# Kernel tuning notes

Hardware: AMD Instinct MI355X
Metric: run time of the kernel (lower is better)

Reference implementation:

```python
import jax, jax.numpy as jnp
import numpy as np

QLEN, MLEN, BSZ = 1024, 1024, 2
D_MODEL, N_HEAD, D_HEAD, D_INNER = 1024, 16, 64, 4096
KLEN = QLEN + MLEN
RLEN = KLEN + QLEN
EPS = 1e-12
SCALE = 1.0 / np.sqrt(D_HEAD).astype(np.float32)
STD = 0.02


def gelu(x):
    # OpenAI-GPT tanh-approx gelu used by XLNet
    return 0.5 * x * (1.0 + jnp.tanh(np.sqrt(2.0 / np.pi) * (x + 0.044715 * x ** 3)))


def layer_norm(x, g, b):
    m = jnp.mean(x, axis=-1, keepdims=True)
    v = jnp.mean((x - m) ** 2, axis=-1, keepdims=True)
    return (x - m) * jax.lax.rsqrt(v + EPS) * g + b


def rel_shift(x, klen):
    # x: [qlen, rlen, bsz, n_head] -> [qlen, klen, bsz, n_head]
    q, r, b, n = x.shape
    x = jnp.reshape(x, (r, q, b, n))[1:]
    x = jnp.reshape(x, (q, r - 1, b, n))[:, :klen]
    return x


def setup_inputs() -> dict:
    key = jax.random.key(0)
    ks = jax.random.split(key, 16)
    h = jax.random.normal(ks[0], (QLEN, BSZ, D_MODEL), jnp.float32)
    mems = jax.random.normal(ks[1], (MLEN, BSZ, D_MODEL), jnp.float32)
    r = jax.random.normal(ks[2], (RLEN, BSZ, D_MODEL), jnp.float32)
    # segment one-hot: 1 if query and key segments differ (XLNet convention)
    qseg = jax.random.randint(ks[3], (QLEN, BSZ), 0, 2)
    kseg = jax.random.randint(ks[4], (KLEN, BSZ), 0, 2)
    seg_mat = jax.nn.one_hot((qseg[:, None, :] != kseg[None, :, :]).astype(jnp.int32), 2, dtype=jnp.float32)  # [q,k,b,2]
    # causal mask with mems: query i may attend to key j <= i + MLEN
    i = jnp.arange(QLEN)[:, None]
    j = jnp.arange(KLEN)[None, :]
    attn_mask = (j > i + MLEN).astype(jnp.float32)[:, :, None, None]  # [q,k,1,1]
    wq = jax.random.normal(ks[5], (D_MODEL, N_HEAD, D_HEAD), jnp.float32) * STD
    wk = jax.random.normal(ks[6], (D_MODEL, N_HEAD, D_HEAD), jnp.float32) * STD
    wv = jax.random.normal(ks[7], (D_MODEL, N_HEAD, D_HEAD), jnp.float32) * STD
    wo = jax.random.normal(ks[8], (D_MODEL, N_HEAD, D_HEAD), jnp.float32) * STD
    wr = jax.random.normal(ks[9], (D_MODEL, N_HEAD, D_HEAD), jnp.float32) * STD
    r_w_bias = jnp.zeros((N_HEAD, D_HEAD), jnp.float32)
    r_r_bias = jnp.zeros((N_HEAD, D_HEAD), jnp.float32)
    r_s_bias = jnp.zeros((N_HEAD, D_HEAD), jnp.float32)
    seg_embed = jax.random.normal(ks[10], (2, N_HEAD, D_HEAD), jnp.float32) * STD
    ln_attn_g = jnp.ones((D_MODEL,), jnp.float32)
    ln_attn_b = jnp.zeros((D_MODEL,), jnp.float32)
    w1 = jax.random.normal(ks[11], (D_MODEL, D_INNER), jnp.float32) * STD
    b1 = jnp.zeros((D_INNER,), jnp.float32)
    w2 = jax.random.normal(ks[12], (D_INNER, D_MODEL), jnp.float32) * STD
    b2 = jnp.zeros((D_MODEL,), jnp.float32)
    ln_ff_g = jnp.ones((D_MODEL,), jnp.float32)
    ln_ff_b = jnp.zeros((D_MODEL,), jnp.float32)
    return dict(h=h, mems=mems, r=r, seg_mat=seg_mat, attn_mask=attn_mask,
                wq=wq, wk=wk, wv=wv, wo=wo, wr=wr,
                r_w_bias=r_w_bias, r_r_bias=r_r_bias, r_s_bias=r_s_bias, seg_embed=seg_embed,
                ln_attn_g=ln_attn_g, ln_attn_b=ln_attn_b,
                w1=w1, b1=b1, w2=w2, b2=b2, ln_ff_g=ln_ff_g, ln_ff_b=ln_ff_b)


def reference(h, mems, r, seg_mat, attn_mask, wq, wk, wv, wo, wr,
              r_w_bias, r_r_bias, r_s_bias, seg_embed,
              ln_attn_g, ln_attn_b, w1, b1, w2, b2, ln_ff_g, ln_ff_b):
    # content-stream XLNet relative attention (g=None path) + FFN
    cat = jnp.concatenate([mems, h], axis=0)            # [klen,b,h]
    q_h = jnp.einsum('ibh,hnd->ibnd', h, wq)
    k_h = jnp.einsum('ibh,hnd->ibnd', cat, wk)
    v_h = jnp.einsum('ibh,hnd->ibnd', cat, wv)
    k_r = jnp.einsum('ibh,hnd->ibnd', r, wr)
    ac = jnp.einsum('ibnd,jbnd->ijbn', q_h + r_w_bias, k_h)
    bd = jnp.einsum('ibnd,jbnd->ijbn', q_h + r_r_bias, k_r)
    bd = rel_shift(bd, KLEN)
    ef = jnp.einsum('ibnd,snd->ibns', q_h + r_s_bias, seg_embed)
    ef = jnp.einsum('ijbs,ibns->ijbn', seg_mat, ef)
    attn_score = (ac + bd + ef) * SCALE - 1e30 * attn_mask
    attn_prob = jax.nn.softmax(attn_score, axis=1)
    attn_vec = jnp.einsum('ijbn,jbnd->ibnd', attn_prob, v_h)
    attn_out = jnp.einsum('ibnd,hnd->ibh', attn_vec, wo) + h
    out_h = layer_norm(attn_out, ln_attn_g, ln_attn_b)
    ff = gelu(out_h @ w1 + b1) @ w2 + b2
    return layer_norm(ff + out_h, ln_ff_g, ln_ff_b)
```

## Files before the change

### kernel.cpp

```cpp
#include <hip/hip_runtime.h>
#include <hip/hip_bf16.h>


#define QLEN 1024
#define MLEN 1024
#define DM 1024
#define NH 16
#define DH 64
#define DI 4096
#define KLEN 2048
#define RLEN 3072

typedef __attribute__((ext_vector_type(8))) short s16x8;
typedef __attribute__((ext_vector_type(4))) float f32x4;
typedef unsigned short us;

__device__ __forceinline__ float bf2f(us u) {
    union { unsigned int i; float f; } x; x.i = ((unsigned int)u) << 16; return x.f;
}
__device__ __forceinline__ us f2bf(float f) {
    union { float f; unsigned int i; } x; x.f = f;
    return (us)((x.i + 0x7fffu + ((x.i >> 16) & 1u)) >> 16);
}
__device__ __forceinline__ void gload16(const void* g, void* lds) {
    __builtin_amdgcn_global_load_lds(
        (const __attribute__((address_space(1))) unsigned int*)g,
        (__attribute__((address_space(3))) unsigned int*)lds, 16, 0, 0);
}

template<bool ISMAX>
__device__ __forceinline__ float block_reduce(float v, float* red, int t) {
    #pragma unroll
    for (int off = 32; off > 0; off >>= 1) {
        float o = __shfl_down(v, off);
        v = ISMAX ? fmaxf(v, o) : (v + o);
    }
    if ((t & 63) == 0) red[t >> 6] = v;
    __syncthreads();
    if (t == 0) {
        float s = red[0];
        #pragma unroll
        for (int w = 1; w < 4; ++w) s = ISMAX ? fmaxf(s, red[w]) : (s + red[w]);
        red[4] = s;
    }
    __syncthreads();
    return red[4];
}

__global__ __launch_bounds__(256) void prep_k(
    const float* __restrict__ mems, const float* __restrict__ h,
    const float* __restrict__ r, const float* __restrict__ wo,
    const float* __restrict__ wq, const float* __restrict__ wk,
    const float* __restrict__ wv, const float* __restrict__ wr,
    const float* __restrict__ w1, const float* __restrict__ w2,
    const float* __restrict__ seg,
    us* __restrict__ cat_bf, us* __restrict__ r_bf, us* __restrict__ wo_b,
    us* __restrict__ wqkv_t, us* __restrict__ wr_t,
    us* __restrict__ w1_t, us* __restrict__ w2_t, us* __restrict__ ksb)
{
    __shared__ us tbuf[64][65];
    int bid = blockIdx.x;
    const int tid = threadIdx.x;
    if (bid < 5632) {
        int t = bid * 256 + tid;
        const float* src; us* dst; int off;
        if (t < 262144)       { src = mems; dst = cat_bf;           off = t; }
        else if (t < 524288)  { src = h;    dst = cat_bf + 2097152; off = t - 262144; }
        else if (t < 1310720) { src = r;    dst = r_bf;             off = t - 524288; }
        else                  { src = wo;   dst = wo_b;             off = t - 1310720; }
        const float4* p = (const float4*)src + 2 * (size_t)off;
        float4 a = p[0], b = p[1];
        us o[8] = { f2bf(a.x), f2bf(a.y), f2bf(a.z), f2bf(a.w),
                    f2bf(b.x), f2bf(b.y), f2bf(b.z), f2bf(b.w) };
        *((uint4*)dst + off) = *(const uint4*)o;
        return;
    }
    bid -= 5632;
    if (bid >= 3072) {
        int t = (bid - 3072) * 256 + tid;
        int bb = t >> 11, j = t & 2047;
        ksb[t] = f2bf(seg[(size_t)j * 4 + bb * 2 + 1]);
        return;
    }
    const float* in; us* out; int R, C, c0, r0;
    if (bid < 1024) {
        int z = bid >> 8, u = bid & 255;
        in  = (z == 0) ? wq : (z == 1) ? wk : (z == 2) ? wv : wr;
        out = (z < 3) ? (wqkv_t + (size_t)z * 1048576) : wr_t;
        R = 1024; C = 1024; c0 = (u & 15) * 64; r0 = (u >> 4) * 64;
    } else if (bid < 2048) {
        int u = bid - 1024;
        in = w1; out = w1_t; R = 1024; C = 4096;
        c0 = (u & 63) * 64; r0 = (u >> 6) * 64;
    } else {
        int u = bid - 2048;
        in = w2; out = w2_t; R = 4096; C = 1024;
        c0 = (u & 15) * 64; r0 = (u >> 4) * 64;
    }
    #pragma unroll
    for (int u = 0; u < 16; ++u) {
        int idx = tid + 256 * u;
        int rr = idx >> 6, cc = idx & 63;
        tbuf[cc][rr] = f2bf(in[(size_t)(r0 + rr) * C + c0 + cc]);
    }
    __syncthreads();
    #pragma unroll
    for (int u = 0; u < 16; ++u) {
        int idx = tid + 256 * u;
        int rr = idx >> 6, cc = idx & 63;
        out[(size_t)(c0 + rr) * R + r0 + cc] = tbuf[rr][cc];
    }
}

__device__ __forceinline__ int offe(int r, int c) {
    return ((r >> 4) * 2 + (c >> 5)) * 512 + (r & 15) * 32 + ((c & 31) ^ ((r & 8) ? 16 : 0));
}

template<int EPI>
__device__ __forceinline__ void gemm8_core(
    const us* __restrict__ A, const us* __restrict__ Bt,
    const float* __restrict__ bias, void* __restrict__ Cout,
    int N, int K, int kbeg, size_t zoff, bool zfirst,
    int bx, int by, us* __restrict__ As8, us* __restrict__ Bs8)
{
    const int tid = threadIdx.x;
    const int w = tid >> 6, l = tid & 63;
    const int lm = l & 15, lg = l >> 4;
    const int wm = w >> 2, wn = w & 3;
    const int m0 = by * 256, n0 = bx * 256;

    int srow[2], scol[2];
    #pragma unroll
    for (int u = 0; u < 2; ++u) {
        int sub = w * 2 + u;
        srow[u] = (sub >> 1) * 16 + (l >> 2);
        scol[u] = (sub & 1) * 32 + (((l & 3) * 8) ^ ((l & 32) ? 16 : 0));
    }

    auto stagePart = [&](int kt1, int P, int db) {
        const us* src = (P < 2) ? (A + (size_t)(m0 + P * 128) * K)
                                : (Bt + (size_t)(n0 + (P - 2) * 128) * K);
        us* dst = ((P < 2) ? As8 : Bs8) + (db * 2 + (P & 1)) * 8192;
        int kc = kbeg + kt1 * 64;
        #pragma unroll
        for (int u = 0; u < 2; ++u)
            gload16(src + (size_t)srow[u] * K + kc + scol[u], dst + (w * 2 + u) * 512);
    };

    f32x4 acc[8][4] = {};
    s16x8 rA0[4][2], rA1[4][2], rB[2][2];

    stagePart(0, 0, 0); stagePart(0, 1, 0); stagePart(0, 2, 0); stagePart(0, 3, 0);

    for (int kt = 0; kt < 16; ++kt) {
        const int d = kt & 1;
        asm volatile("s_waitcnt vmcnt(0)" ::: "memory");
        __builtin_amdgcn_s_barrier();
        asm volatile("" ::: "memory");
        const bool hn = (kt + 1 < 16);
        const us* Ab = As8 + (d * 2 + wm) * 8192;
        const us* Bb = Bs8 + (d * 2 + (wn >> 1)) * 8192;

        if (hn) stagePart(kt + 1, 0, d ^ 1);
        #pragma unroll
        for (int mf2 = 0; mf2 < 4; ++mf2)
            #pragma unroll
            for (int kk = 0; kk < 2; ++kk)
                rA0[mf2][kk] = *(const s16x8*)&Ab[offe(mf2 * 16 + lm, kk * 32 + lg * 8)];
        #pragma unroll
        for (int nf2 = 0; nf2 < 2; ++nf2)
            #pragma unroll
            for (int kk = 0; kk < 2; ++kk)
                rB[nf2][kk] = *(const s16x8*)&Bb[offe((wn & 1) * 64 + nf2 * 16 + lm, kk * 32 + lg * 8)];
        __builtin_amdgcn_s_setprio(1);
        #pragma unroll
        for (int mf2 = 0; mf2 < 4; ++mf2)
            #pragma unroll
            for (int nf2 = 0; nf2 < 2; ++nf2)
                #pragma unroll
                for (int kk = 0; kk < 2; ++kk)
                    acc[mf2][nf2] = __builtin_amdgcn_mfma_f32_16x16x32_bf16(
                        rA0[mf2][kk], rB[nf2][kk], acc[mf2][nf2], 0, 0, 0);
        __builtin_amdgcn_s_setprio(0);

        if (hn) stagePart(kt + 1, 1, d ^ 1);
        #pragma unroll
        for (int mf2 = 0; mf2 < 4; ++mf2)
            #pragma unroll
            for (int kk = 0; kk < 2; ++kk)
                rA1[mf2][kk] = *(const s16x8*)&Ab[offe(64 + mf2 * 16 + lm, kk * 32 + lg * 8)];
        __builtin_amdgcn_s_setprio(1);
        #pragma unroll
        for (int mf2 = 0; mf2 < 4; ++mf2)
            #pragma unroll
            for (int nf2 = 0; nf2 < 2; ++nf2)
                #pragma unroll
                for (int kk = 0; kk < 2; ++kk)
                    acc[4 + mf2][nf2] = __builtin_amdgcn_mfma_f32_16x16x32_bf16(
                        rA1[mf2][kk], rB[nf2][kk], acc[4 + mf2][nf2], 0, 0, 0);
        __builtin_amdgcn_s_setprio(0);

        if (hn) stagePart(kt + 1, 2, d ^ 1);
        #pragma unroll
        for (int nf2 = 0; nf2 < 2; ++nf2)
            #pragma unroll
            for (int kk = 0; kk < 2; ++kk)
                rB[nf2][kk] = *(const s16x8*)&Bb[offe((wn & 1) * 64 + (2 + nf2) * 16 + lm, kk * 32 + lg * 8)];
        __builtin_amdgcn_s_setprio(1);
        #pragma unroll
        for (int mf2 = 0; mf2 < 4; ++mf2)
            #pragma unroll
            for (int nf2 = 0; nf2 < 2; ++nf2)
                #pragma unroll
                for (int kk = 0; kk < 2; ++kk)
                    acc[4 + mf2][2 + nf2] = __builtin_amdgcn_mfma_f32_16x16x32_bf16(
                        rA1[mf2][kk], rB[nf2][kk], acc[4 + mf2][2 + nf2], 0, 0, 0);
        __builtin_amdgcn_s_setprio(0);

        if (hn) stagePart(kt + 1, 3, d ^ 1);
        __builtin_amdgcn_s_setprio(1);
        #pragma unroll
        for (int mf2 = 0; mf2 < 4; ++mf2)
            #pragma unroll
            for (int nf2 = 0; nf2 < 2; ++nf2)
                #pragma unroll
                for (int kk = 0; kk < 2; ++kk)
                    acc[mf2][2 + nf2] = __builtin_amdgcn_mfma_f32_16x16x32_bf16(
                        rA0[mf2][kk], rB[nf2][kk], acc[mf2][2 + nf2], 0, 0, 0);
        __builtin_amdgcn_s_setprio(0);
    }

    #pragma unroll
    for (int mf = 0; mf < 8; ++mf) {
        #pragma unroll
        for (int nf = 0; nf < 4; ++nf) {
            #pragma unroll
            for (int rr = 0; rr < 4; ++rr) {
                int row = m0 + wm * 128 + mf * 16 + lg * 4 + rr;
                int col = n0 + wn * 64 + nf * 16 + lm;
                float v = acc[mf][nf][rr];
                if (EPI == 3) {
                    int s = row >> 1, bb = row & 1, nn = col >> 6, dd = col & 63;
                    if (s >= 1) {
                        int g = (s - 1) >> 4, lmw = (s - 1) & 15;
                        int ks2 = dd >> 5, lg2 = (dd >> 3) & 3, e2 = dd & 7;
                        ((us*)Cout)[((((size_t)(bb * 16 + nn)) * 144 + g) * 2 + ks2) * 512
                                    + (lg2 * 16 + lmw) * 8 + e2] = f2bf(v);
                    }
                } else {
                    int which = col >> 10;
                    int nn = (col >> 6) & 15, dd = col & 63, bb = row & 1;
                    us val = f2bf(v);
                    us* base = (us*)Cout;
                    if (which == 0) {
                        if (row >= 2048)
                            base[(((size_t)(bb * 16 + nn)) * 1024 + ((row - 2048) >> 1)) * 64 + dd] = val;
                    } else if (which == 1) {
                        int j = row >> 1;
                        int jt = j >> 6, ff = (j >> 4) & 3, lmw = j & 15;
                        int ks2 = dd >> 5, lg2 = (dd >> 3) & 3, e2 = dd & 7;
                        (base + 2097152)[((((size_t)(bb * 16 + nn)) * 32 + jt) * 8 + ff * 2 + ks2) * 512
                                         + (lg2 * 16 + lmw) * 8 + e2] = val;
                    } else {
                        int j = row >> 1;
                        int jt = j >> 6, ks2 = (j >> 5) & 1, lg2 = (j >> 3) & 3, e2 = j & 7;
                        int df = dd >> 4, lmw = dd & 15;
                        (base + 6291456)[((((size_t)(bb * 16 + nn)) * 32 + jt) * 8 + df * 2 + ks2) * 512
                                         + (lg2 * 16 + lmw) * 8 + e2] = val;
                    }
                }
            }
        }
    }
}

__global__ __launch_bounds__(512) void proj8_k(
    const us* __restrict__ cat_bf, const us* __restrict__ wqkv_t,
    const us* __restrict__ r_bf, const us* __restrict__ wr_t,
    us* __restrict__ qkv_out, us* __restrict__ krf_out)
{
    __shared__ __align__(16) us As8[2 * 2 * 8192];
    __shared__ __align__(16) us Bs8[2 * 2 * 8192];
    int bid = blockIdx.x;
    if (bid < 192) {
        int swz = (bid & 7) * 24 + (bid >> 3);
        gemm8_core<4>(cat_bf, wqkv_t, nullptr, qkv_out, 3072, 1024, 0,
                      0, true, swz % 12, swz / 12, As8, Bs8);
    } else {
        int idx = bid - 192;
        gemm8_core<3>(r_bf, wr_t, nullptr, krf_out, 1024, 1024, 0,
                      0, true, idx & 3, idx >> 2, As8, Bs8);
    }
}

template<int TM, int EPI>
__device__ __forceinline__ void gemm_core(
    const us* __restrict__ A, const us* __restrict__ Bt,
    const float* __restrict__ bias, void* __restrict__ Cout,
    int N, int K, int kbeg, int kchunk, size_t zoff, bool zfirst,
    int bx, int by, us* __restrict__ As, us* __restrict__ Bs)
{
    constexpr int MF = TM / 32;
    constexpr int AISS = TM / 64;
    const int tid = threadIdx.x;
    const int w = tid >> 6, l = tid & 63;
    const int lm = l & 15, lg = l >> 4;
    const int m0 = by * TM, n0 = bx * 128;
    const int wr = (w >> 1) * (TM / 2), wc = (w & 1) * 64;
    const int nt = kchunk / 32;

    f32x4 acc[MF][4] = {};

    auto stage = [&](int buf, int k0) {
        #pragma unroll
        for (int u = 0; u < AISS; ++u) {
            int c = (u * 4 + w) * 64 + l;
            int row = c & (TM - 1), kc = c >> (TM == 128 ? 7 : 6);
            gload16(A + (size_t)(m0 + row) * K + k0 + kc * 8,
                    As + buf * (TM * 32) + (u * 4 + w) * 512);
        }
        #pragma unroll
        for (int u = 0; u < 2; ++u) {
            int c = (u * 4 + w) * 64 + l;
            int row = c & 127, kc = c >> 7;
            gload16(Bt + (size_t)(n0 + row) * K + k0 + kc * 8,
                    Bs + buf * 4096 + (u * 4 + w) * 512);
        }
    };

    stage(0, kbeg);
    int cur = 0;
    for (int t = 0; t < nt; ++t) {
        asm volatile("s_waitcnt vmcnt(0)" ::: "memory");
        __builtin_amdgcn_s_barrier();
        asm volatile("" ::: "memory");
        if (t + 1 < nt) stage(cur ^ 1, kbeg + (t + 1) * 32);

        s16x8 af[MF], bfr[4];
        #pragma unroll
        for (int mf = 0; mf < MF; ++mf)
            af[mf] = *(const s16x8*)&As[cur * (TM * 32) + (lg * TM + wr + mf * 16 + lm) * 8];
        #pragma unroll
        for (int nf = 0; nf < 4; ++nf)
            bfr[nf] = *(const s16x8*)&Bs[cur * 4096 + (lg * 128 + wc + nf * 16 + lm) * 8];
        #pragma unroll
        for (int mf = 0; mf < MF; ++mf)
            #pragma unroll
            for (int nf = 0; nf < 4; ++nf)
                acc[mf][nf] = __builtin_amdgcn_mfma_f32_16x16x32_bf16(
                    af[mf], bfr[nf], acc[mf][nf], 0, 0, 0);
        cur ^= 1;
    }

    #pragma unroll
    for (int mf = 0; mf < MF; ++mf) {
        #pragma unroll
        for (int nf = 0; nf < 4; ++nf) {
            #pragma unroll
            for (int rr = 0; rr < 4; ++rr) {
                int row = m0 + wr + mf * 16 + lg * 4 + rr;
                int col = n0 + wc + nf * 16 + lm;
                float v = acc[mf][nf][rr];
                if (EPI == 1 || (EPI == 2 && zfirst)) v += bias[col];
                if (EPI == 1) {
                    float targ = 0.7978845608028654f * (v + 0.044715f * v * v * v);
                    v = 0.5f * v * (1.0f + tanhf(targ));
                    ((us*)Cout)[(size_t)row * N + col] = f2bf(v);
                } else {
                    ((float*)Cout + zoff)[(size_t)row * N + col] = v;
                }
            }
        }
    }
}

template<int TM, int EPI>
__global__ __launch_bounds__(256) void gemm2(
    const us* __restrict__ A, const us* __restrict__ Bt,
    const float* __restrict__ bias, void* __restrict__ Cout,
    int N, int K, int kchunk, size_t zstride)
{
    __shared__ us As[2 * TM * 32];
    __shared__ us Bs[2 * 128 * 32];
    int lin = blockIdx.y * gridDim.x + blockIdx.x;
    int nwg = gridDim.x * gridDim.y;
    int swz = (lin & 7) * (nwg >> 3) + (lin >> 3);
    int bx = swz % gridDim.x, by = swz / gridDim.x;
    gemm_core<TM, EPI>(A, Bt, bias, Cout, N, K, blockIdx.z * kchunk, kchunk,
                       (size_t)blockIdx.z * zstride, blockIdx.z == 0, bx, by, As, Bs);
}

__global__ __launch_bounds__(256) void attn9_k(
    const us* __restrict__ qb, const us* __restrict__ kfr, const us* __restrict__ vfr,
    const us* __restrict__ krf, const us* __restrict__ ksb,
    const float* __restrict__ rwb, const float* __restrict__ rrb,
    const float* __restrict__ rsb, const float* __restrict__ se,
    const float* __restrict__ seg,
    us* __restrict__ av)
{
    __shared__ float G_lds[4 * 80 * 20];
    __shared__ us P_lds[4 * 16 * 64];
    __shared__ us KS_lds[2048];
    __shared__ float Qx_lds[64][2];

    const int tid = threadIdx.x;
    const int w = tid >> 6, l = tid & 63;
    const int lm = l & 15, lg = l >> 4;
    int lin = blockIdx.x;
    int p = lin >> 1, parity = lin & 1;
    const int bn = p >> 3;
    int q = p & 7;
    const int i0t = parity ? (15 - q) : q;
    const int i0 = i0t * 64;
    const int b = bn >> 4, n = bn & 15;
    const int i = i0 + w * 16 + lm;

    const float SC = 0.125f * 1.44269504088896340736f;

    const us* kbase = kfr + (size_t)bn * 131072;
    const us* vbase = vfr + (size_t)bn * 131072;
    const us* krbase = krf + (size_t)bn * 147456;

    gload16(ksb + b * KLEN + (w * 64 + l) * 8, &KS_lds[w * 512]);
    {
        const us* qrow = qb + ((size_t)bn * QLEN + i0 + l) * DH;
        s16x8 qv8[8];
        #pragma unroll
        for (int c = 0; c < 8; ++c) qv8[c] = *(const s16x8*)(qrow + c * 8);
        float e0 = 0.f, e1 = 0.f;
        #pragma unroll
        for (int c = 0; c < 8; ++c)
            #pragma unroll
            for (int e = 0; e < 8; ++e) {
                int d = c * 8 + e;
                float qv = bf2f((us)qv8[c][e]) + rsb[n * DH + d];
                e0 = fmaf(qv, se[(0 * NH + n) * DH + d], e0);
                e1 = fmaf(qv, se[(1 * NH + n) * DH + d], e1);
            }
        float qsI = seg[(size_t)(i0 + l) * 8192 + b * 2 + 1];
        float qs0 = seg[b * 2 + 1];
        float qs = (qsI != qs0) ? 1.f : 0.f;
        float ed = e1 - e0;
        if (w == 0) {
            Qx_lds[l][0] = (e0 + qs * ed) * SC;
            Qx_lds[l][1] = ed * (1.f - 2.f * qs) * SC;
        }
    }
    asm volatile("s_waitcnt vmcnt(0)" ::: "memory");
    __syncthreads();

    s16x8 qwf[2], qrf[2], qxf;
    {
        const us* qrow = qb + ((size_t)bn * QLEN + i) * DH;
        #pragma unroll
        for (int ks = 0; ks < 2; ++ks) {
            s16x8 v = *(const s16x8*)(qrow + ks * 32 + lg * 8);
            #pragma unroll
            for (int e = 0; e < 8; ++e) {
                int d = ks * 32 + lg * 8 + e;
                float f = bf2f((us)v[e]);
                qwf[ks][e] = (short)f2bf((f + rwb[n * DH + d]) * SC);
                qrf[ks][e] = (short)f2bf((f + rrb[n * DH + d]) * SC);
            }
        }
        #pragma unroll
        for (int e = 0; e < 8; ++e) qxf[e] = 0;
        if (lg == 0) {
            qxf[0] = (short)f2bf(Qx_lds[w * 16 + lm][0]);
            qxf[1] = (short)f2bf(Qx_lds[w * 16 + lm][1]);
        }
    }

    int njt = ((i0 + 63 + MLEN) >> 6) + 1;
    if (njt > 32) njt = 32;
    const int gq = 63 - (i0 >> 4) - w;

    f32x4 of[4] = {{0,0,0,0},{0,0,0,0},{0,0,0,0},{0,0,0,0}};
    float M = -3.0e38f, L = 0.f;
    float* gw = &G_lds[w * 1600];
    us* pw = &P_lds[w * 1024];

    for (int jt = 0; jt < njt; ++jt) {
        const int j0 = jt * 64;

        s16x8 kf[4][2], vf[4][2];
        #pragma unroll
        for (int f = 0; f < 4; ++f) {
            #pragma unroll
            for (int ks = 0; ks < 2; ++ks) {
                kf[f][ks] = *(const s16x8*)(kbase + (size_t)(((jt * 4 + f) * 2 + ks) * 64 + l) * 8);
                vf[f][ks] = *(const s16x8*)(vbase + (size_t)(((jt * 4 + f) * 2 + ks) * 64 + l) * 8);
            }
        }

        __builtin_amdgcn_s_setprio(1);
        #pragma unroll
        for (int pf = 0; pf < 5; ++pf) {
            int g = gq + 4 * jt + pf;
            f32x4 gacc = {0, 0, 0, 0};
            #pragma unroll
            for (int ks = 0; ks < 2; ++ks) {
                s16x8 a = *(const s16x8*)(krbase + (size_t)((g * 2 + ks) * 64 + l) * 8);
                gacc = __builtin_amdgcn_mfma_f32_16x16x32_bf16(a, qrf[ks], gacc, 0, 0, 0);
            }
            #pragma unroll
            for (int rr = 0; rr < 4; ++rr)
                gw[(pf * 16 + lg * 4 + rr) * 20 + lm] = gacc[rr];
        }
        f32x4 sf[4];
        #pragma unroll
        for (int f = 0; f < 4; ++f) {
            f32x4 cfr = {0, 0, 0, 0};
            cfr = __builtin_amdgcn_mfma_f32_16x16x32_bf16(kf[f][0], qwf[0], cfr, 0, 0, 0);
            cfr = __builtin_amdgcn_mfma_f32_16x16x32_bf16(kf[f][1], qwf[1], cfr, 0, 0, 0);
            s16x8 aext;
            #pragma unroll
            for (int e = 0; e < 8; ++e) aext[e] = 0;
            if (lg == 0) {
                aext[0] = (short)0x3F80;
                aext[1] = (short)KS_lds[j0 + f * 16 + lm];
            }
            cfr = __builtin_amdgcn_mfma_f32_16x16x32_bf16(aext, qxf, cfr, 0, 0, 0);
            sf[f] = cfr;
        }
        __builtin_amdgcn_s_setprio(0);

        float sv[16];
        #pragma unroll
        for (int f = 0; f < 4; ++f)
            #pragma unroll
            for (int rr = 0; rr < 4; ++rr) {
                int jl = f * 16 + lg * 4 + rr;
                sv[f * 4 + rr] = sf[f][rr] + gw[(jl + 15 - lm) * 20 + lm];
            }
        if (j0 + 63 > i0 + w * 16 + MLEN) {
            #pragma unroll
            for (int f = 0; f < 4; ++f)
                #pragma unroll
                for (int rr = 0; rr < 4; ++rr) {
                    int jl = f * 16 + lg * 4 + rr;
                    if (j0 + jl > i + MLEN) sv[f * 4 + rr] = -1.0e30f;
                }
        }
        float tmax = sv[0];
        #pragma unroll
        for (int u = 1; u < 16; ++u) tmax = fmaxf(tmax, sv[u]);
        tmax = fmaxf(tmax, __shfl_xor(tmax, 16));
        tmax = fmaxf(tmax, __shfl_xor(tmax, 32));
        float Mnew = fmaxf(M, tmax);
        float scale;
        asm("v_exp_f32 %0, %1" : "=v"(scale) : "v"(M - Mnew));
        float psum = 0.f;
        unsigned int pk[8];
        #pragma unroll
        for (int f = 0; f < 4; ++f) {
            #pragma unroll
            for (int rp = 0; rp < 2; ++rp) {
                float p0, p1;
                asm("v_exp_f32 %0, %1" : "=v"(p0) : "v"(sv[f * 4 + rp * 2] - Mnew));
                asm("v_exp_f32 %0, %1" : "=v"(p1) : "v"(sv[f * 4 + rp * 2 + 1] - Mnew));
                psum += p0 + p1;
                unsigned int pkv;
                asm("v_cvt_pk_bf16_f32 %0, %1, %2" : "=v"(pkv) : "v"(p0), "v"(p1));
                pk[f * 2 + rp] = pkv;
            }
        }
        psum += __shfl_xor(psum, 16);
        psum += __shfl_xor(psum, 32);
        L = L * scale + psum;
        M = Mnew;
        float rs4[4];
        #pragma unroll
        for (int rr = 0; rr < 4; ++rr)
            rs4[rr] = __shfl(scale, (l & 48) | (lg * 4 + rr));
        #pragma unroll
        for (int df = 0; df < 4; ++df)
            #pragma unroll
            for (int rr = 0; rr < 4; ++rr)
                of[df][rr] *= rs4[rr];
        #pragma unroll
        for (int f = 0; f < 4; ++f) {
            #pragma unroll
            for (int rp = 0; rp < 2; ++rp) {
                int jl2 = f * 16 + lg * 4 + rp * 2;
                *(unsigned int*)&pw[lm * 64 + (((jl2 * 2) ^ ((lm & 7) << 4)) >> 1)] = pk[f * 2 + rp];
            }
        }
        __builtin_amdgcn_s_setprio(1);
        #pragma unroll
        for (int ks = 0; ks < 2; ++ks) {
            s16x8 pa = *(const s16x8*)&pw[lm * 64 + (((ks * 64 + lg * 16) ^ ((lm & 7) << 4)) >> 1)];
            #pragma unroll
            for (int df = 0; df < 4; ++df)
                of[df] = __builtin_amdgcn_mfma_f32_16x16x32_bf16(pa, vf[df][ks], of[df], 0, 0, 0);
        }
        __builtin_amdgcn_s_setprio(0);
    }

    float rl4[4];
    #pragma unroll
    for (int rr = 0; rr < 4; ++rr)
        rl4[rr] = __shfl(L, (l & 48) | (lg * 4 + rr));
    #pragma unroll
    for (int df = 0; df < 4; ++df) {
        #pragma unroll
        for (int rr = 0; rr < 4; ++rr) {
            int m2 = lg * 4 + rr;
            int d = df * 16 + lm;
            int irow = i0 + w * 16 + m2;
            av[((size_t)irow * 2 + b) * DM + n * DH + d] = f2bf(of[df][rr] / rl4[rr]);
        }
    }
}

template<int NSUM, bool RESBF, bool OUTBF>
__global__ __launch_bounds__(256) void ln_k(
    const float* __restrict__ a, const void* __restrict__ resid,
    const float* __restrict__ g, const float* __restrict__ bb,
    void* __restrict__ out)
{
    __shared__ float xs[DM];
    __shared__ float red[5];
    const int r = blockIdx.x;
    const int t = threadIdx.x;
    float lsum = 0.f;
    #pragma unroll
    for (int u = 0; u < 4; ++u) {
        int hdx = t + 256 * u;
        float x = RESBF ? bf2f(((const us*)resid)[(size_t)r * DM + hdx])
                        : ((const float*)resid)[(size_t)r * DM + hdx];
        #pragma unroll
        for (int s = 0; s < NSUM; ++s)
            x += a[(size_t)s * 2097152 + (size_t)r * DM + hdx];
        xs[hdx] = x;
        lsum += x;
    }
    float m = block_reduce<false>(lsum, red, t) * (1.0f / DM);
    float lv = 0.f;
    #pragma unroll
    for (int u = 0; u < 4; ++u) {
        int hdx = t + 256 * u;
        float dd = xs[hdx] - m;
        lv += dd * dd;
    }
    float var = block_reduce<false>(lv, red, t) * (1.0f / DM);
    float rs = rsqrtf(var + 1e-12f);
    #pragma unroll
    for (int u = 0; u < 4; ++u) {
        int hdx = t + 256 * u;
        float y = (xs[hdx] - m) * rs * g[hdx] + bb[hdx];
        if (OUTBF) ((us*)out)[(size_t)r * DM + hdx] = f2bf(y);
        else       ((float*)out)[(size_t)r * DM + hdx] = y;
    }
}

extern "C" void kernel_launch(void* const* d_in, const int* in_sizes, int n_in,
                              void* d_out, int out_size, void* d_ws, size_t ws_size,
                              hipStream_t stream) {
    const float* h         = (const float*)d_in[0];
    const float* mems      = (const float*)d_in[1];
    const float* r         = (const float*)d_in[2];
    const float* seg_mat   = (const float*)d_in[3];
    const float* wq        = (const float*)d_in[5];
    const float* wk        = (const float*)d_in[6];
    const float* wv        = (const float*)d_in[7];
    const float* wo        = (const float*)d_in[8];
    const float* wr        = (const float*)d_in[9];
    const float* rwb       = (const float*)d_in[10];
    const float* rrb       = (const float*)d_in[11];
    const float* rsb       = (const float*)d_in[12];
    const float* seg_embed = (const float*)d_in[13];
    const float* ln_g      = (const float*)d_in[14];
    const float* ln_b      = (const float*)d_in[15];
    const float* w1        = (const float*)d_in[16];
    const float* b1        = (const float*)d_in[17];
    const float* w2        = (const float*)d_in[18];
    const float* b2        = (const float*)d_in[19];
    const float* lf_g      = (const float*)d_in[20];
    const float* lf_b      = (const float*)d_in[21];
    float* out = (float*)d_out;
    char* W = (char*)d_ws;
    const size_t MB = 1ull << 20;

    us*    cat_bf = (us*)(W);
    us*    r_bf   = (us*)(W + 8  * MB);
    us*    wqkv_t = (us*)(W + 20 * MB);
    us*    wr_t   = (us*)(W + 26 * MB);
    us*    wo_b   = (us*)(W + 28 * MB);
    us*    w1_t   = (us*)(W + 30 * MB);
    us*    w2_t   = (us*)(W + 38 * MB);
    us*    q_bf   = (us*)(W + 46 * MB);
    us*    kfrag  = q_bf + 2097152;
    us*    vfrag  = q_bf + 6291456;
    us*    krf    = (us*)(W + 66 * MB);
    us*    av_bf  = (us*)(W + 78 * MB);
    us*    ks_bf  = (us*)(W + 82 * MB);
    us*    oh_bf  = (us*)(W + 83 * MB);
    float* ao     = (float*)(W + 8 * MB);
    us*    ff1_bf = (us*)(W + 46 * MB);
    float* ff2    = (float*)(W);

    dim3 blk(256);
    dim3 blk8(512);
    prep_k<<<dim3(8720), blk, 0, stream>>>(mems, h, r, wo, wq, wk, wv, wr, w1, w2, seg_mat,
                                           cat_bf, r_bf, wo_b, wqkv_t, wr_t, w1_t, w2_t, ks_bf);
    proj8_k<<<dim3(264), blk8, 0, stream>>>(cat_bf, wqkv_t, r_bf, wr_t, q_bf, krf);
    attn9_k<<<dim3(512), blk, 0, stream>>>(q_bf, kfrag, vfrag, krf, ks_bf,
                                           rwb, rrb, rsb, seg_embed, seg_mat, av_bf);
    gemm2<64, 0><<<dim3(8, 32, 2), blk, 0, stream>>>(av_bf, wo_b, nullptr, ao, 1024, 1024, 512, 2097152);
    ln_k<2, false, true><<<dim3(2048), blk, 0, stream>>>(ao, h, ln_g, ln_b, oh_bf);
    gemm2<128, 1><<<dim3(32, 16), blk, 0, stream>>>(oh_bf, w1_t, b1, ff1_bf, 4096, 1024, 1024, 0);
    gemm2<64, 2><<<dim3(8, 32, 4), blk, 0, stream>>>(ff1_bf, w2_t, b2, ff2, 1024, 4096, 1024, 2097152);
    ln_k<4, true, false><<<dim3(2048), blk, 0, stream>>>(ff2, oh_bf, lf_g, lf_b, out);
}
```

Before: 307.2 us.

## Double-buffer attention tile loads, defer softmax rescale, reorder blocks longest-first

The attention kernel now prefetches the next key/value/relative-key fragments into a second register set while computing the current tile, so global loads overlap with MFMA work. The online softmax skips the running-max update and the output rescale when every lane's new max stays within a threshold of the old one (an FA4-style lazy rescale). Block scheduling changes from parity-interleaved to heaviest query tiles first. The extra buffers raise register pressure, which may lower occupancy, and the lazy rescale lets exponentials grow up to about 2^11.5 before renormalising.

```diff
diff --git a/kernel.cpp b/kernel.cpp
--- a/kernel.cpp
+++ b/kernel.cpp
@@ -390,7 +390,7 @@
                        (size_t)blockIdx.z * zstride, blockIdx.z == 0, bx, by, As, Bs);
 }
 
-__global__ __launch_bounds__(256) void attn9_k(
+__global__ __launch_bounds__(256) void attn10_k(
     const us* __restrict__ qb, const us* __restrict__ kfr, const us* __restrict__ vfr,
     const us* __restrict__ krf, const us* __restrict__ ksb,
     const float* __restrict__ rwb, const float* __restrict__ rrb,
@@ -407,15 +407,14 @@
     const int w = tid >> 6, l = tid & 63;
     const int lm = l & 15, lg = l >> 4;
     int lin = blockIdx.x;
-    int p = lin >> 1, parity = lin & 1;
-    const int bn = p >> 3;
-    int q = p & 7;
-    const int i0t = parity ? (15 - q) : q;
+    const int i0t = 15 - (lin >> 5);
+    const int bn = lin & 31;
     const int i0 = i0t * 64;
     const int b = bn >> 4, n = bn & 15;
     const int i = i0 + w * 16 + lm;
 
     const float SC = 0.125f * 1.44269504088896340736f;
+    const float THR = 11.5416f;
 
     const us* kbase = kfr + (size_t)bn * 131072;
     const us* vbase = vfr + (size_t)bn * 131072;
@@ -480,29 +479,30 @@
     float* gw = &G_lds[w * 1600];
     us* pw = &P_lds[w * 1024];
 
-    for (int jt = 0; jt < njt; ++jt) {
-        const int j0 = jt * 64;
-
-        s16x8 kf[4][2], vf[4][2];
-        #pragma unroll
-        for (int f = 0; f < 4; ++f) {
+    auto loadT = [&](s16x8 (&kf)[4][2], s16x8 (&vf)[4][2], s16x8 (&kr)[5][2], int jt) {
+        #pragma unroll
+        for (int f = 0; f < 4; ++f)
             #pragma unroll
             for (int ks = 0; ks < 2; ++ks) {
                 kf[f][ks] = *(const s16x8*)(kbase + (size_t)(((jt * 4 + f) * 2 + ks) * 64 + l) * 8);
                 vf[f][ks] = *(const s16x8*)(vbase + (size_t)(((jt * 4 + f) * 2 + ks) * 64 + l) * 8);
             }
-        }
-
-        __builtin_amdgcn_s_setprio(1);
         #pragma unroll
         for (int pf = 0; pf < 5; ++pf) {
             int g = gq + 4 * jt + pf;
+            #pragma unroll
+            for (int ks = 0; ks < 2; ++ks)
+                kr[pf][ks] = *(const s16x8*)(krbase + (size_t)((g * 2 + ks) * 64 + l) * 8);
+        }
+    };
+
+    auto computeT = [&](s16x8 (&kf)[4][2], s16x8 (&vf)[4][2], s16x8 (&kr)[5][2], int j0) {
+        __builtin_amdgcn_s_setprio(1);
+        #pragma unroll
+        for (int pf = 0; pf < 5; ++pf) {
             f32x4 gacc = {0, 0, 0, 0};
-            #pragma unroll
-            for (int ks = 0; ks < 2; ++ks) {
-                s16x8 a = *(const s16x8*)(krbase + (size_t)((g * 2 + ks) * 64 + l) * 8);
-                gacc = __builtin_amdgcn_mfma_f32_16x16x32_bf16(a, qrf[ks], gacc, 0, 0, 0);
-            }
+            gacc = __builtin_amdgcn_mfma_f32_16x16x32_bf16(kr[pf][0], qrf[0], gacc, 0, 0, 0);
+            gacc = __builtin_amdgcn_mfma_f32_16x16x32_bf16(kr[pf][1], qrf[1], gacc, 0, 0, 0);
             #pragma unroll
             for (int rr = 0; rr < 4; ++rr)
                 gw[(pf * 16 + lg * 4 + rr) * 20 + lm] = gacc[rr];
@@ -547,9 +547,9 @@
         for (int u = 1; u < 16; ++u) tmax = fmaxf(tmax, sv[u]);
         tmax = fmaxf(tmax, __shfl_xor(tmax, 16));
         tmax = fmaxf(tmax, __shfl_xor(tmax, 32));
-        float Mnew = fmaxf(M, tmax);
-        float scale;
-        asm("v_exp_f32 %0, %1" : "=v"(scale) : "v"(M - Mnew));
+
+        const bool defer = __all(tmax - M <= THR);
+        float Mnew = defer ? M : fmaxf(M, tmax);
         float psum = 0.f;
         unsigned int pk[8];
         #pragma unroll
@@ -567,17 +567,23 @@
         }
         psum += __shfl_xor(psum, 16);
         psum += __shfl_xor(psum, 32);
-        L = L * scale + psum;
-        M = Mnew;
-        float rs4[4];
-        #pragma unroll
-        for (int rr = 0; rr < 4; ++rr)
-            rs4[rr] = __shfl(scale, (l & 48) | (lg * 4 + rr));
-        #pragma unroll
-        for (int df = 0; df < 4; ++df)
+        if (defer) {
+            L += psum;
+        } else {
+            float scale;
+            asm("v_exp_f32 %0, %1" : "=v"(scale) : "v"(M - Mnew));
+            L = L * scale + psum;
+            M = Mnew;
+            float rs4[4];
             #pragma unroll
             for (int rr = 0; rr < 4; ++rr)
-                of[df][rr] *= rs4[rr];
+                rs4[rr] = __shfl(scale, (l & 48) | (lg * 4 + rr));
+            #pragma unroll
+            for (int df = 0; df < 4; ++df)
+                #pragma unroll
+                for (int rr = 0; rr < 4; ++rr)
+                    of[df][rr] *= rs4[rr];
+        }
         #pragma unroll
         for (int f = 0; f < 4; ++f) {
             #pragma unroll
@@ -595,6 +601,20 @@
                 of[df] = __builtin_amdgcn_mfma_f32_16x16x32_bf16(pa, vf[df][ks], of[df], 0, 0, 0);
         }
         __builtin_amdgcn_s_setprio(0);
+    };
+
+    s16x8 kfA[4][2], vfA[4][2], krA[5][2];
+    s16x8 kfB[4][2], vfB[4][2], krB[5][2];
+    loadT(kfA, vfA, krA, 0);
+    for (int jt = 0; jt < njt; ++jt) {
+        const bool hn = (jt + 1 < njt);
+        if ((jt & 1) == 0) {
+            if (hn) loadT(kfB, vfB, krB, jt + 1);
+            computeT(kfA, vfA, krA, jt * 64);
+        } else {
+            if (hn) loadT(kfA, vfA, krA, jt + 1);
+            computeT(kfB, vfB, krB, jt * 64);
+        }
     }
 
     float rl4[4];
@@ -705,8 +725,8 @@
     prep_k<<<dim3(8720), blk, 0, stream>>>(mems, h, r, wo, wq, wk, wv, wr, w1, w2, seg_mat,
                                            cat_bf, r_bf, wo_b, wqkv_t, wr_t, w1_t, w2_t, ks_bf);
     proj8_k<<<dim3(264), blk8, 0, stream>>>(cat_bf, wqkv_t, r_bf, wr_t, q_bf, krf);
-    attn9_k<<<dim3(512), blk, 0, stream>>>(q_bf, kfrag, vfrag, krf, ks_bf,
-                                           rwb, rrb, rsb, seg_embed, seg_mat, av_bf);
+    attn10_k<<<dim3(512), blk, 0, stream>>>(q_bf, kfrag, vfrag, krf, ks_bf,
+                                            rwb, rrb, rsb, seg_embed, seg_mat, av_bf);
     gemm2<64, 0><<<dim3(8, 32, 2), blk, 0, stream>>>(av_bf, wo_b, nullptr, ao, 1024, 1024, 512, 2097152);
     ln_k<2, false, true><<<dim3(2048), blk, 0, stream>>>(ao, h, ln_g, ln_b, oh_bf);
     gemm2<128, 1><<<dim3(32, 16), blk, 0, stream>>>(oh_bf, w1_t, b1, ff1_bf, 4096, 1024, 1024, 0);
```

Result: slower. 329.9 us (+7.4%).

## Split attention key range in two halves with separate combine kernel

Applied to the files above, without the earlier changes.

The attention kernel now splits each query tile's key loop into two halves run by separate workgroups, doubling the grid from 512 to 1024 blocks. Each half writes unnormalized fp32 partial outputs plus running max and sum, and a new combine kernel merges the halves with log-sum-exp rescaling into the bf16 attention vector. This targets poor occupancy and load imbalance on a 256-CU device, at the cost of extra fp32 partial traffic, an extra launch, and repeated per-block Q setup. The earlier parity-based tile pairing for balancing causal work is dropped.

```diff
diff --git a/kernel.cpp b/kernel.cpp
--- a/kernel.cpp
+++ b/kernel.cpp
@@ -390,13 +390,13 @@
                        (size_t)blockIdx.z * zstride, blockIdx.z == 0, bx, by, As, Bs);
 }
 
-__global__ __launch_bounds__(256) void attn9_k(
+__global__ __launch_bounds__(256) void attn11_k(
     const us* __restrict__ qb, const us* __restrict__ kfr, const us* __restrict__ vfr,
     const us* __restrict__ krf, const us* __restrict__ ksb,
     const float* __restrict__ rwb, const float* __restrict__ rrb,
     const float* __restrict__ rsb, const float* __restrict__ se,
     const float* __restrict__ seg,
-    us* __restrict__ av)
+    float* __restrict__ po, float* __restrict__ pm, float* __restrict__ pl)
 {
     __shared__ float G_lds[4 * 80 * 20];
     __shared__ us P_lds[4 * 16 * 64];
@@ -407,10 +407,9 @@
     const int w = tid >> 6, l = tid & 63;
     const int lm = l & 15, lg = l >> 4;
     int lin = blockIdx.x;
-    int p = lin >> 1, parity = lin & 1;
-    const int bn = p >> 3;
-    int q = p & 7;
-    const int i0t = parity ? (15 - q) : q;
+    const int half = lin >> 9;
+    const int i0t = (lin >> 5) & 15;
+    const int bn = lin & 31;
     const int i0 = i0t * 64;
     const int b = bn >> 4, n = bn & 15;
     const int i = i0 + w * 16 + lm;
@@ -473,6 +472,9 @@
 
     int njt = ((i0 + 63 + MLEN) >> 6) + 1;
     if (njt > 32) njt = 32;
+    const int nj0 = (njt + 1) >> 1;
+    const int jbeg = half ? nj0 : 0;
+    const int jend = half ? njt : nj0;
     const int gq = 63 - (i0 >> 4) - w;
 
     f32x4 of[4] = {{0,0,0,0},{0,0,0,0},{0,0,0,0},{0,0,0,0}};
@@ -480,7 +482,7 @@
     float* gw = &G_lds[w * 1600];
     us* pw = &P_lds[w * 1024];
 
-    for (int jt = 0; jt < njt; ++jt) {
+    for (int jt = jbeg; jt < jend; ++jt) {
         const int j0 = jt * 64;
 
         s16x8 kf[4][2], vf[4][2];
@@ -597,20 +599,58 @@
         __builtin_amdgcn_s_setprio(0);
     }
 
-    float rl4[4];
-    #pragma unroll
-    for (int rr = 0; rr < 4; ++rr)
+    const int pidx = (half * 16 + i0t) * 32 + bn;
+    float rl4[4], rm4[4];
+    #pragma unroll
+    for (int rr = 0; rr < 4; ++rr) {
         rl4[rr] = __shfl(L, (l & 48) | (lg * 4 + rr));
+        rm4[rr] = __shfl(M, (l & 48) | (lg * 4 + rr));
+    }
     #pragma unroll
     for (int df = 0; df < 4; ++df) {
         #pragma unroll
         for (int rr = 0; rr < 4; ++rr) {
-            int m2 = lg * 4 + rr;
-            int d = df * 16 + lm;
-            int irow = i0 + w * 16 + m2;
-            av[((size_t)irow * 2 + b) * DM + n * DH + d] = f2bf(of[df][rr] / rl4[rr]);
-        }
-    }
+            int rloc = w * 16 + lg * 4 + rr;
+            po[((size_t)pidx * 64 + rloc) * 64 + df * 16 + lm] = of[df][rr];
+        }
+    }
+    if (lm == 0) {
+        #pragma unroll
+        for (int rr = 0; rr < 4; ++rr) {
+            int rloc = w * 16 + lg * 4 + rr;
+            pm[pidx * 64 + rloc] = rm4[rr];
+            pl[pidx * 64 + rloc] = rl4[rr];
+        }
+    }
+}
+
+__global__ __launch_bounds__(256) void avcomb_k(
+    const float* __restrict__ po, const float* __restrict__ pm,
+    const float* __restrict__ pl, us* __restrict__ av)
+{
+    const int avrow = blockIdx.x;
+    const int t = threadIdx.x;
+    const int i = avrow >> 1, b = avrow & 1;
+    const int i0t = i >> 6, rl = i & 63;
+    const int col0 = t * 4;
+    const int n = col0 >> 6, d0 = col0 & 63;
+    const int bn = b * 16 + n;
+    const int p0 = (0 + i0t) * 32 + bn;
+    const int p1 = (16 + i0t) * 32 + bn;
+    float M0 = pm[p0 * 64 + rl], M1 = pm[p1 * 64 + rl];
+    float L0 = pl[p0 * 64 + rl], L1 = pl[p1 * 64 + rl];
+    float Mx = fmaxf(M0, M1);
+    float s0, s1;
+    asm("v_exp_f32 %0, %1" : "=v"(s0) : "v"(M0 - Mx));
+    asm("v_exp_f32 %0, %1" : "=v"(s1) : "v"(M1 - Mx));
+    float inv = 1.0f / (L0 * s0 + L1 * s1);
+    float4 o0 = *(const float4*)&po[((size_t)p0 * 64 + rl) * 64 + d0];
+    float4 o1 = *(const float4*)&po[((size_t)p1 * 64 + rl) * 64 + d0];
+    us o[4] = { f2bf((o0.x * s0 + o1.x * s1) * inv),
+                f2bf((o0.y * s0 + o1.y * s1) * inv),
+                f2bf((o0.z * s0 + o1.z * s1) * inv),
+                f2bf((o0.w * s0 + o1.w * s1) * inv) };
+    *(unsigned long long*)&av[(size_t)avrow * 1024 + col0] = *(const unsigned long long*)o;
 }
 
 template<int NSUM, bool RESBF, bool OUTBF>
@@ -696,6 +736,9 @@
     us*    av_bf  = (us*)(W + 78 * MB);
     us*    ks_bf  = (us*)(W + 82 * MB);
     us*    oh_bf  = (us*)(W + 83 * MB);
+    float* po     = (float*)(W + 8 * MB);
+    float* pm     = (float*)(W + 24 * MB);
+    float* pl     = (float*)(W + 24 * MB + 512 * 1024);
     float* ao     = (float*)(W + 8 * MB);
     us*    ff1_bf = (us*)(W + 46 * MB);
     float* ff2    = (float*)(W);
@@ -705,8 +748,9 @@
     prep_k<<<dim3(8720), blk, 0, stream>>>(mems, h, r, wo, wq, wk, wv, wr, w1, w2, seg_mat,
                                            cat_bf, r_bf, wo_b, wqkv_t, wr_t, w1_t, w2_t, ks_bf);
     proj8_k<<<dim3(264), blk8, 0, stream>>>(cat_bf, wqkv_t, r_bf, wr_t, q_bf, krf);
-    attn9_k<<<dim3(512), blk, 0, stream>>>(q_bf, kfrag, vfrag, krf, ks_bf,
-                                           rwb, rrb, rsb, seg_embed, seg_mat, av_bf);
+    attn11_k<<<dim3(1024), blk, 0, stream>>>(q_bf, kfrag, vfrag, krf, ks_bf,
+                                             rwb, rrb, rsb, seg_embed, seg_mat, po, pm, pl);
+    avcomb_k<<<dim3(2048), blk, 0, stream>>>(po, pm, pl, av_bf);
     gemm2<64, 0><<<dim3(8, 32, 2), blk, 0, stream>>>(av_bf, wo_b, nullptr, ao, 1024, 1024, 512, 2097152);
     ln_k<2, false, true><<<dim3(2048), blk, 0, stream>>>(ao, h, ln_g, ln_b, oh_bf);
     gemm2<128, 1><<<dim3(32, 16), blk, 0, stream>>>(oh_bf, w1_t, b1, ff1_bf, 4096, 1024, 1024, 0);
```

Result: no change. 307.1 us (-0.0%).
